# Performance work log

Hardware: AMD Instinct MI355X
Metric: run time of the kernel (lower is better)

The kernel has to match this reference:

```python
import jax, jax.numpy as jnp
import numpy as np

N_NODES = 100000
N_EDGES = 1600000
IN_FEATS = 256
HEADS = 4
OUT_FEATS = 32


def setup_inputs() -> dict:
    key = jax.random.key(0)
    k1, k2, k3, k4, k5, k6 = jax.random.split(key, 6)
    feat = jax.random.normal(k1, (N_NODES, IN_FEATS), dtype=jnp.float32)
    fc_w = jax.random.normal(k2, (HEADS * OUT_FEATS, IN_FEATS), dtype=jnp.float32) * (1.0 / np.sqrt(IN_FEATS))
    attn_l = jax.random.normal(k3, (1, HEADS, OUT_FEATS), dtype=jnp.float32) * 0.1
    attn_r = jax.random.normal(k4, (1, HEADS, OUT_FEATS), dtype=jnp.float32) * 0.1
    src = jax.random.randint(k5, (N_EDGES,), 0, N_NODES, dtype=jnp.int32)
    dst = jax.random.randint(k6, (N_EDGES,), 0, N_NODES, dtype=jnp.int32)
    return {"feat": feat, "fc_w": fc_w, "attn_l": attn_l, "attn_r": attn_r, "src": src, "dst": dst}


def reference(feat, fc_w, attn_l, attn_r, src, dst):
    # feat: [N, F_in]; fc_w: [H*D, F_in]; attn_l/r: [1, H, D]; src/dst: [E]
    N = feat.shape[0]
    H, D = attn_l.shape[1], attn_l.shape[2]
    # linear projection (no bias), viewed as [N, H, D]
    ft = (feat @ fc_w.T).reshape(N, H, D)
    # per-node attention logits
    el = jnp.einsum('nhd,hd->nh', ft, attn_l[0])  # [N, H]
    er = jnp.einsum('nhd,hd->nh', ft, attn_r[0])  # [N, H]
    # per-edge score: leaky_relu(el[src] + er[dst])
    e = jax.nn.leaky_relu(el[src] + er[dst], negative_slope=0.2)  # [E, H]
    # edge softmax over incoming edges of each dst node (stable)
    emax = jax.ops.segment_max(e, dst, num_segments=N)  # [N, H]
    a = jnp.exp(e - emax[dst])  # [E, H]
    asum = jax.ops.segment_sum(a, dst, num_segments=N)  # [N, H]
    a = a / asum[dst]
    # attn_drop is a no-op in eval mode; weighted scatter-sum aggregation
    msg = ft[src] * a[:, :, None]  # [E, H, D]
    out = jax.ops.segment_sum(msg, dst, num_segments=N)  # [N, H, D]
    # final_layer=False, activation=None, norm=None -> flatten heads
    return out.reshape(N, H * D)
```

## Files before the change

kernel.cpp:

```cpp
#include <hip/hip_runtime.h>
#include <hip/hip_bf16.h>
#include <float.h>

#define IN_F 256
#define HD   128
#define NH   4
#define GM   128

typedef __bf16 bf16x8 __attribute__((ext_vector_type(8)));
typedef __bf16 bf16x2 __attribute__((ext_vector_type(2)));
typedef float  f32x4  __attribute__((ext_vector_type(4)));

__device__ __forceinline__ bf16x8 cvt8(const float4 a, const float4 b) {
    bf16x8 r;
    r[0] = (__bf16)a.x; r[1] = (__bf16)a.y; r[2] = (__bf16)a.z; r[3] = (__bf16)a.w;
    r[4] = (__bf16)b.x; r[5] = (__bf16)b.y; r[6] = (__bf16)b.z; r[7] = (__bf16)b.w;
    return r;
}

__global__ __launch_bounds__(256) void gemm_ft_mfma(const float* __restrict__ feat,
                                                    const float* __restrict__ w,
                                                    __bf16* __restrict__ ft,
                                                    int N, int ntiles) {
    __shared__ __align__(16) __bf16 Bs[128][264];
    __shared__ __align__(16) __bf16 As[GM][40];
    const int t = threadIdx.x;
    const int wv = t >> 6;
    const int lane = t & 63;

    {
        const int col = t >> 1;
        const int koff = (t & 1) * 128;
        const float* wp = w + (size_t)col * IN_F + koff;
#pragma unroll
        for (int i = 0; i < 128; i += 8) {
            const float4 v0 = *(const float4*)(wp + i);
            const float4 v1 = *(const float4*)(wp + i + 4);
            *(bf16x8*)&Bs[col][koff + i] = cvt8(v0, v1);
        }
    }

    const int ar = t >> 1;
    const int ac = (t & 1) * 16;
    const int frow = lane & 15;
    const int fk   = (lane >> 4) * 8;

    for (int tile = blockIdx.x; tile < ntiles; tile += gridDim.x) {
        const int row0 = tile * GM;
        f32x4 acc[2][8];
#pragma unroll
        for (int mt = 0; mt < 2; ++mt)
#pragma unroll
            for (int ct = 0; ct < 8; ++ct) acc[mt][ct] = {0.f, 0.f, 0.f, 0.f};

        for (int ks = 0; ks < 8; ++ks) {
            const int k0 = ks * 32;
            __syncthreads();
            bf16x8 av0, av1;
            const int gr = row0 + ar;
            if (gr < N) {
                const float* fp = feat + (size_t)gr * IN_F + k0 + ac;
                const float4 v0 = *(const float4*)(fp);
                const float4 v1 = *(const float4*)(fp + 4);
                const float4 v2 = *(const float4*)(fp + 8);
                const float4 v3 = *(const float4*)(fp + 12);
                av0 = cvt8(v0, v1);
                av1 = cvt8(v2, v3);
            } else {
#pragma unroll
                for (int i = 0; i < 8; ++i) { av0[i] = (__bf16)0.f; av1[i] = (__bf16)0.f; }
            }
            *(bf16x8*)&As[ar][ac] = av0;
            *(bf16x8*)&As[ar][ac + 8] = av1;
            __syncthreads();

            const bf16x8 af0 = *(const bf16x8*)&As[wv * 32 + frow][fk];
            const bf16x8 af1 = *(const bf16x8*)&As[wv * 32 + 16 + frow][fk];
#pragma unroll
            for (int ct = 0; ct < 8; ++ct) {
                const bf16x8 bfrag = *(const bf16x8*)&Bs[ct * 16 + frow][k0 + fk];
                acc[0][ct] = __builtin_amdgcn_mfma_f32_16x16x32_bf16(af0, bfrag, acc[0][ct], 0, 0, 0);
                acc[1][ct] = __builtin_amdgcn_mfma_f32_16x16x32_bf16(af1, bfrag, acc[1][ct], 0, 0, 0);
            }
        }
        const int rb = row0 + wv * 32 + (lane >> 4) * 4;
#pragma unroll
        for (int mt = 0; mt < 2; ++mt)
#pragma unroll
            for (int ct = 0; ct < 8; ++ct)
#pragma unroll
                for (int reg = 0; reg < 4; ++reg) {
                    const int m = rb + mt * 16 + reg;
                    if (m < N) ft[(size_t)m * HD + ct * 16 + frow] = (__bf16)acc[mt][ct][reg];
                }
    }
}

__global__ __launch_bounds__(256) void eler_k(const __bf16* __restrict__ ft,
                                              const float* __restrict__ attn_l,
                                              const float* __restrict__ attn_r,
                                              float* __restrict__ el,
                                              float* __restrict__ er, int N) {
    const int lane = threadIdx.x & 63;
    const int node = blockIdx.x * 4 + (threadIdx.x >> 6);
    if (node >= N) return;
    const bf16x2 f  = *(const bf16x2*)(ft + (size_t)node * HD + lane * 2);
    const float2 al = *(const float2*)(attn_l + lane * 2);
    const float2 ar = *(const float2*)(attn_r + lane * 2);
    const float fx = (float)f[0], fy = (float)f[1];
    float pl = fx * al.x + fy * al.y;
    float pr = fx * ar.x + fy * ar.y;
#pragma unroll
    for (int s = 1; s < 16; s <<= 1) {
        pl += __shfl_xor(pl, s);
        pr += __shfl_xor(pr, s);
    }
    if ((lane & 15) == 0) {
        const int h = lane >> 4;
        el[(size_t)node * NH + h] = pl;
        er[(size_t)node * NH + h] = pr;
    }
}

__global__ __launch_bounds__(256) void deg_rank_k(const int* __restrict__ dst,
                                                  int* __restrict__ deg,
                                                  int* __restrict__ rank, int E) {
    const int i = blockIdx.x * 256 + threadIdx.x;
    if (i < E) rank[i] = atomicAdd(&deg[dst[i]], 1);
}

__global__ __launch_bounds__(1024) void scan1_k(const int* __restrict__ deg,
                                                int* __restrict__ off,
                                                int* __restrict__ bsum, int N) {
    __shared__ int lds[1024];
    const int t = threadIdx.x;
    const int g = blockIdx.x * 1024 + t;
    const int x = (g < N) ? deg[g] : 0;
    lds[t] = x;
    __syncthreads();
    int v = x;
    for (int s = 1; s < 1024; s <<= 1) {
        const int add = (t >= s) ? lds[t - s] : 0;
        __syncthreads();
        v += add;
        lds[t] = v;
        __syncthreads();
    }
    if (g < N) off[g] = v - x;
    if (t == 1023) bsum[blockIdx.x] = v;
}

__global__ __launch_bounds__(128) void scan2_k(const int* __restrict__ bsum,
                                               int* __restrict__ boff, int nb) {
    __shared__ int lds[128];
    const int t = threadIdx.x;
    const int x = (t < nb) ? bsum[t] : 0;
    lds[t] = x;
    __syncthreads();
    int v = x;
    for (int s = 1; s < 128; s <<= 1) {
        const int add = (t >= s) ? lds[t - s] : 0;
        __syncthreads();
        v += add;
        lds[t] = v;
        __syncthreads();
    }
    boff[t] = v - x;
}

__global__ __launch_bounds__(256) void scatter_k(const int* __restrict__ src,
                                                 const int* __restrict__ dst,
                                                 const int* __restrict__ off,
                                                 const int* __restrict__ boff,
                                                 const int* __restrict__ rank,
                                                 int* __restrict__ ssrc, int E) {
    const int i = blockIdx.x * 256 + threadIdx.x;
    if (i < E) {
        const int d = dst[i];
        const int p = off[d] + boff[d >> 10] + rank[i];
        ssrc[p] = src[i];
    }
}

__global__ __launch_bounds__(64) void aggregate_k(const __bf16* __restrict__ ft,
                                                  const float* __restrict__ el,
                                                  const float* __restrict__ er,
                                                  const int* __restrict__ deg,
                                                  const int* __restrict__ off,
                                                  const int* __restrict__ boff,
                                                  const int* __restrict__ ssrc,
                                                  float* __restrict__ out, int N) {
    const int n = blockIdx.x;
    const int lane = threadIdx.x;
    const int il = lane & 15;
    const int q  = lane >> 4;
    const int h  = il >> 2;
    float4* outp = (float4*)(out + (size_t)n * HD);
    const int dn = deg[n];
    if (dn == 0) {
        if (q < 2) outp[il * 2 + q] = make_float4(0.f, 0.f, 0.f, 0.f);
        return;
    }
    const int start = off[n] + boff[n >> 10];
    const float4 er4 = *(const float4*)(er + (size_t)n * NH);

    __shared__ float a_lds[64 * NH];
    __shared__ int   s_lds[64];
    float4 ssum = make_float4(0.f, 0.f, 0.f, 0.f);
    float acc[8];
#pragma unroll
    for (int i = 0; i < 8; ++i) acc[i] = 0.f;

    for (int c0 = 0; c0 < dn; c0 += 64) {
        const int j = c0 + lane;
        float4 a = make_float4(0.f, 0.f, 0.f, 0.f);
        int sv = 0;
        if (j < dn) {
            sv = ssrc[start + j];
            float4 e = *(const float4*)(el + (size_t)sv * NH);
            e.x += er4.x; e.y += er4.y; e.z += er4.z; e.w += er4.w;
            e.x = e.x >= 0.f ? e.x : 0.2f * e.x;
            e.y = e.y >= 0.f ? e.y : 0.2f * e.y;
            e.z = e.z >= 0.f ? e.z : 0.2f * e.z;
            e.w = e.w >= 0.f ? e.w : 0.2f * e.w;
            a.x = __expf(e.x); a.y = __expf(e.y);
            a.z = __expf(e.z); a.w = __expf(e.w);
            ssum.x += a.x; ssum.y += a.y; ssum.z += a.z; ssum.w += a.w;
        }
        s_lds[lane] = sv;
        *(float4*)(a_lds + lane * NH) = a;
        __syncthreads();
        const int cnt = min(64, dn - c0);
        for (int j2 = 0; j2 < cnt; j2 += 8) {
            const int e0 = j2 + q;
            const int e1 = j2 + 4 + q;
            const int sv0 = s_lds[e0];
            const int sv1 = s_lds[e1];
            const float a0 = a_lds[e0 * NH + h];
            const float a1 = a_lds[e1 * NH + h];
            const bf16x8 f0 = *(const bf16x8*)(ft + (size_t)sv0 * HD + il * 8);
            const bf16x8 f1 = *(const bf16x8*)(ft + (size_t)sv1 * HD + il * 8);
#pragma unroll
            for (int k = 0; k < 8; ++k) acc[k] = fmaf(a0, (float)f0[k], acc[k]);
#pragma unroll
            for (int k = 0; k < 8; ++k) acc[k] = fmaf(a1, (float)f1[k], acc[k]);
        }
        __syncthreads();
    }
#pragma unroll
    for (int s = 1; s < 64; s <<= 1) {
        ssum.x += __shfl_xor(ssum.x, s);
        ssum.y += __shfl_xor(ssum.y, s);
        ssum.z += __shfl_xor(ssum.z, s);
        ssum.w += __shfl_xor(ssum.w, s);
    }
#pragma unroll
    for (int k = 0; k < 8; ++k) {
        acc[k] += __shfl_xor(acc[k], 16);
        acc[k] += __shfl_xor(acc[k], 32);
    }
    const float sumh = (h == 0) ? ssum.x : (h == 1) ? ssum.y : (h == 2) ? ssum.z : ssum.w;
    const float inv = 1.f / sumh;
    if (q < 2) {
        const int b = q * 4;
        outp[il * 2 + q] = make_float4(acc[b] * inv, acc[b + 1] * inv,
                                       acc[b + 2] * inv, acc[b + 3] * inv);
    }
}

extern "C" void kernel_launch(void* const* d_in, const int* in_sizes, int n_in,
                              void* d_out, int out_size, void* d_ws, size_t ws_size,
                              hipStream_t stream) {
    const float* feat   = (const float*)d_in[0];
    const float* fc_w   = (const float*)d_in[1];
    const float* attn_l = (const float*)d_in[2];
    const float* attn_r = (const float*)d_in[3];
    const int*   src    = (const int*)d_in[4];
    const int*   dst    = (const int*)d_in[5];
    const int N = in_sizes[0] / IN_F;
    const int E = in_sizes[4];
    float* out = (float*)d_out;

    char* wp = (char*)d_ws;
    __bf16* ft = (__bf16*)wp; wp += (size_t)N * HD * 2;
    float* el  = (float*)wp; wp += (size_t)N * NH * 4;
    float* er  = (float*)wp; wp += (size_t)N * NH * 4;
    int* deg   = (int*)wp;   wp += (size_t)N * 4;
    int* off   = (int*)wp;   wp += (size_t)N * 4;
    int* bsum  = (int*)wp;   wp += 1024;
    int* boff  = (int*)wp;   wp += 1024;
    int* rank  = (int*)wp;   wp += (size_t)E * 4;
    int* ssrc  = (int*)wp;   wp += (size_t)E * 4;

    hipMemsetAsync(deg, 0, (size_t)N * 4, stream);

    const int ntiles = (N + GM - 1) / GM;
    gemm_ft_mfma<<<dim3(512), dim3(256), 0, stream>>>(feat, fc_w, ft, N, ntiles);
    eler_k<<<dim3((N + 3) / 4), dim3(256), 0, stream>>>(ft, attn_l, attn_r, el, er, N);
    deg_rank_k<<<dim3((E + 255) / 256), dim3(256), 0, stream>>>(dst, deg, rank, E);
    const int nblk = (N + 1023) >> 10;
    scan1_k<<<dim3(nblk), dim3(1024), 0, stream>>>(deg, off, bsum, N);
    scan2_k<<<dim3(1), dim3(128), 0, stream>>>(bsum, boff, nblk);
    scatter_k<<<dim3((E + 255) / 256), dim3(256), 0, stream>>>(src, dst, off, boff, rank, ssrc, E);
    aggregate_k<<<dim3(N), dim3(64), 0, stream>>>(ft, el, er, deg, off, boff, ssrc, out, N);
}
```

Baseline: 385.9 us.

## Fuse attention logits into LDS-free GEMM, warp-shuffle scan, unroll aggregation gathers

Weights are pre-converted once into bf16 MFMA fragment order by a small prep kernel. The projection GEMM then reads A fragments straight from global memory, with no LDS staging and no barriers, and computes el/er in its epilogue from the fp32 accumulators. This removes the separate eler kernel and its reread of ft. The block scan now uses wavefront shuffles instead of a barrier-heavy LDS Hillis-Steele loop, and the aggregation loop gathers four neighbor rows per step instead of two to raise memory-level parallelism. The risks are redundant global reads of feat and weight fragments across waves, and extra register pressure.

```diff
diff --git a/kernel.cpp b/kernel.cpp
--- a/kernel.cpp
+++ b/kernel.cpp
@@ -5,7 +5,6 @@
 #define IN_F 256
 #define HD   128
 #define NH   4
-#define GM   128
 
 typedef __bf16 bf16x8 __attribute__((ext_vector_type(8)));
 typedef __bf16 bf16x2 __attribute__((ext_vector_type(2)));
@@ -18,107 +17,108 @@
     return r;
 }
 
-__global__ __launch_bounds__(256) void gemm_ft_mfma(const float* __restrict__ feat,
-                                                    const float* __restrict__ w,
-                                                    __bf16* __restrict__ ft,
-                                                    int N, int ntiles) {
-    __shared__ __align__(16) __bf16 Bs[128][264];
-    __shared__ __align__(16) __bf16 As[GM][40];
+__global__ __launch_bounds__(256) void wprep_k(const float* __restrict__ w,
+                                               __bf16* __restrict__ wfrag) {
+    const int idx = blockIdx.x * 256 + threadIdx.x;
+    const int lane = idx & 63;
+    const int ct = (idx >> 6) & 7;
+    const int ks = idx >> 9;
+    const float* p = w + (size_t)(ct * 16 + (lane & 15)) * IN_F + ks * 32 + (lane >> 4) * 8;
+    const float4 v0 = *(const float4*)p;
+    const float4 v1 = *(const float4*)(p + 4);
+    *(bf16x8*)&wfrag[(size_t)idx * 8] = cvt8(v0, v1);
+}
+
+__global__ __launch_bounds__(256) void gemm_ft_fused(const float* __restrict__ feat,
+                                                     const __bf16* __restrict__ wfrag,
+                                                     const float* __restrict__ attn_l,
+                                                     const float* __restrict__ attn_r,
+                                                     __bf16* __restrict__ ft,
+                                                     float* __restrict__ el,
+                                                     float* __restrict__ er, int N) {
     const int t = threadIdx.x;
     const int wv = t >> 6;
     const int lane = t & 63;
-
-    {
-        const int col = t >> 1;
-        const int koff = (t & 1) * 128;
-        const float* wp = w + (size_t)col * IN_F + koff;
-#pragma unroll
-        for (int i = 0; i < 128; i += 8) {
-            const float4 v0 = *(const float4*)(wp + i);
-            const float4 v1 = *(const float4*)(wp + i + 4);
-            *(bf16x8*)&Bs[col][koff + i] = cvt8(v0, v1);
-        }
-    }
-
-    const int ar = t >> 1;
-    const int ac = (t & 1) * 16;
-    const int frow = lane & 15;
-    const int fk   = (lane >> 4) * 8;
-
-    for (int tile = blockIdx.x; tile < ntiles; tile += gridDim.x) {
-        const int row0 = tile * GM;
-        f32x4 acc[2][8];
-#pragma unroll
-        for (int mt = 0; mt < 2; ++mt)
-#pragma unroll
-            for (int ct = 0; ct < 8; ++ct) acc[mt][ct] = {0.f, 0.f, 0.f, 0.f};
-
-        for (int ks = 0; ks < 8; ++ks) {
-            const int k0 = ks * 32;
-            __syncthreads();
-            bf16x8 av0, av1;
-            const int gr = row0 + ar;
-            if (gr < N) {
-                const float* fp = feat + (size_t)gr * IN_F + k0 + ac;
-                const float4 v0 = *(const float4*)(fp);
-                const float4 v1 = *(const float4*)(fp + 4);
-                const float4 v2 = *(const float4*)(fp + 8);
-                const float4 v3 = *(const float4*)(fp + 12);
-                av0 = cvt8(v0, v1);
-                av1 = cvt8(v2, v3);
+    const int il = lane & 15;
+    const int fk = (lane >> 4) * 8;
+    const int rbase = blockIdx.x * 128 + wv * 32;
+
+    f32x4 acc[2][8];
+#pragma unroll
+    for (int mt = 0; mt < 2; ++mt)
+#pragma unroll
+        for (int ct = 0; ct < 8; ++ct) acc[mt][ct] = {0.f, 0.f, 0.f, 0.f};
+
+    const int r0 = rbase + il;
+    const int r1 = rbase + 16 + il;
+
+    for (int ks = 0; ks < 8; ++ks) {
+        bf16x8 af0, af1;
+        {
+            if (r0 < N) {
+                const float* p = feat + (size_t)r0 * IN_F + ks * 32 + fk;
+                af0 = cvt8(*(const float4*)p, *(const float4*)(p + 4));
             } else {
 #pragma unroll
-                for (int i = 0; i < 8; ++i) { av0[i] = (__bf16)0.f; av1[i] = (__bf16)0.f; }
-            }
-            *(bf16x8*)&As[ar][ac] = av0;
-            *(bf16x8*)&As[ar][ac + 8] = av1;
-            __syncthreads();
-
-            const bf16x8 af0 = *(const bf16x8*)&As[wv * 32 + frow][fk];
-            const bf16x8 af1 = *(const bf16x8*)&As[wv * 32 + 16 + frow][fk];
-#pragma unroll
-            for (int ct = 0; ct < 8; ++ct) {
-                const bf16x8 bfrag = *(const bf16x8*)&Bs[ct * 16 + frow][k0 + fk];
-                acc[0][ct] = __builtin_amdgcn_mfma_f32_16x16x32_bf16(af0, bfrag, acc[0][ct], 0, 0, 0);
-                acc[1][ct] = __builtin_amdgcn_mfma_f32_16x16x32_bf16(af1, bfrag, acc[1][ct], 0, 0, 0);
-            }
-        }
-        const int rb = row0 + wv * 32 + (lane >> 4) * 4;
-#pragma unroll
-        for (int mt = 0; mt < 2; ++mt)
+                for (int i = 0; i < 8; ++i) af0[i] = (__bf16)0.f;
+            }
+            if (r1 < N) {
+                const float* p = feat + (size_t)r1 * IN_F + ks * 32 + fk;
+                af1 = cvt8(*(const float4*)p, *(const float4*)(p + 4));
+            } else {
+#pragma unroll
+                for (int i = 0; i < 8; ++i) af1[i] = (__bf16)0.f;
+            }
+        }
+        const bf16x8* bp = (const bf16x8*)&wfrag[(size_t)(ks * 8) * 512 + lane * 8];
+#pragma unroll
+        for (int ct = 0; ct < 8; ++ct) {
+            const bf16x8 bfrag = bp[ct * 64];
+            acc[0][ct] = __builtin_amdgcn_mfma_f32_16x16x32_bf16(af0, bfrag, acc[0][ct], 0, 0, 0);
+            acc[1][ct] = __builtin_amdgcn_mfma_f32_16x16x32_bf16(af1, bfrag, acc[1][ct], 0, 0, 0);
+        }
+    }
+
+    float AL[8], AR[8];
+#pragma unroll
+    for (int ct = 0; ct < 8; ++ct) {
+        AL[ct] = attn_l[ct * 16 + il];
+        AR[ct] = attn_r[ct * 16 + il];
+    }
+
+    const int rquad = (lane >> 4) * 4;
+#pragma unroll
+    for (int mt = 0; mt < 2; ++mt) {
+#pragma unroll
+        for (int reg = 0; reg < 4; ++reg) {
+            const int row = rbase + mt * 16 + rquad + reg;
 #pragma unroll
             for (int ct = 0; ct < 8; ++ct)
-#pragma unroll
-                for (int reg = 0; reg < 4; ++reg) {
-                    const int m = rb + mt * 16 + reg;
-                    if (m < N) ft[(size_t)m * HD + ct * 16 + frow] = (__bf16)acc[mt][ct][reg];
+                if (row < N) ft[(size_t)row * HD + ct * 16 + il] = (__bf16)acc[mt][ct][reg];
+            float pl[NH], pr[NH];
+#pragma unroll
+            for (int h = 0; h < NH; ++h) {
+                const float v0 = acc[mt][2 * h][reg], v1 = acc[mt][2 * h + 1][reg];
+                pl[h] = v0 * AL[2 * h] + v1 * AL[2 * h + 1];
+                pr[h] = v0 * AR[2 * h] + v1 * AR[2 * h + 1];
+            }
+#pragma unroll
+            for (int s = 1; s < 16; s <<= 1) {
+#pragma unroll
+                for (int h = 0; h < NH; ++h) {
+                    pl[h] += __shfl_xor(pl[h], s);
+                    pr[h] += __shfl_xor(pr[h], s);
                 }
-    }
-}
-
-__global__ __launch_bounds__(256) void eler_k(const __bf16* __restrict__ ft,
-                                              const float* __restrict__ attn_l,
-                                              const float* __restrict__ attn_r,
-                                              float* __restrict__ el,
-                                              float* __restrict__ er, int N) {
-    const int lane = threadIdx.x & 63;
-    const int node = blockIdx.x * 4 + (threadIdx.x >> 6);
-    if (node >= N) return;
-    const bf16x2 f  = *(const bf16x2*)(ft + (size_t)node * HD + lane * 2);
-    const float2 al = *(const float2*)(attn_l + lane * 2);
-    const float2 ar = *(const float2*)(attn_r + lane * 2);
-    const float fx = (float)f[0], fy = (float)f[1];
-    float pl = fx * al.x + fy * al.y;
-    float pr = fx * ar.x + fy * ar.y;
-#pragma unroll
-    for (int s = 1; s < 16; s <<= 1) {
-        pl += __shfl_xor(pl, s);
-        pr += __shfl_xor(pr, s);
-    }
-    if ((lane & 15) == 0) {
-        const int h = lane >> 4;
-        el[(size_t)node * NH + h] = pl;
-        er[(size_t)node * NH + h] = pr;
+            }
+            if (il < 8 && row < N) {
+                const int h = il & 3;
+                const float v = (h == 0) ? ((il < 4) ? pl[0] : pr[0])
+                              : (h == 1) ? ((il < 4) ? pl[1] : pr[1])
+                              : (h == 2) ? ((il < 4) ? pl[2] : pr[2])
+                                         : ((il < 4) ? pl[3] : pr[3]);
+                ((il < 4) ? el : er)[(size_t)row * NH + h] = v;
+            }
+        }
     }
 }
 
@@ -132,22 +132,33 @@
 __global__ __launch_bounds__(1024) void scan1_k(const int* __restrict__ deg,
                                                 int* __restrict__ off,
                                                 int* __restrict__ bsum, int N) {
-    __shared__ int lds[1024];
+    __shared__ int wsum[16];
     const int t = threadIdx.x;
+    const int lane = t & 63;
+    const int wid = t >> 6;
     const int g = blockIdx.x * 1024 + t;
     const int x = (g < N) ? deg[g] : 0;
-    lds[t] = x;
+    int v = x;
+#pragma unroll
+    for (int s = 1; s < 64; s <<= 1) {
+        const int u = __shfl_up(v, s);
+        if (lane >= s) v += u;
+    }
+    if (lane == 63) wsum[wid] = v;
     __syncthreads();
-    int v = x;
-    for (int s = 1; s < 1024; s <<= 1) {
-        const int add = (t >= s) ? lds[t - s] : 0;
-        __syncthreads();
-        v += add;
-        lds[t] = v;
-        __syncthreads();
-    }
-    if (g < N) off[g] = v - x;
-    if (t == 1023) bsum[blockIdx.x] = v;
+    if (t < 16) {
+        int wv_ = wsum[t];
+#pragma unroll
+        for (int s = 1; s < 16; s <<= 1) {
+            const int u = __shfl_up(wv_, s);
+            if (t >= s) wv_ += u;
+        }
+        wsum[t] = wv_;
+    }
+    __syncthreads();
+    const int woff = wid ? wsum[wid - 1] : 0;
+    if (g < N) off[g] = woff + v - x;
+    if (t == 1023) bsum[blockIdx.x] = wsum[15];
 }
 
 __global__ __launch_bounds__(128) void scan2_k(const int* __restrict__ bsum,
@@ -230,20 +241,24 @@
         s_lds[lane] = sv;
         *(float4*)(a_lds + lane * NH) = a;
         __syncthreads();
-        const int cnt = min(64, dn - c0);
-        for (int j2 = 0; j2 < cnt; j2 += 8) {
-            const int e0 = j2 + q;
-            const int e1 = j2 + 4 + q;
-            const int sv0 = s_lds[e0];
-            const int sv1 = s_lds[e1];
-            const float a0 = a_lds[e0 * NH + h];
-            const float a1 = a_lds[e1 * NH + h];
+        const int cnt16 = (min(64, dn - c0) + 15) & ~15;
+        for (int j2 = 0; j2 < cnt16; j2 += 16) {
+            const int e0 = j2 + q, e1 = j2 + 4 + q, e2 = j2 + 8 + q, e3 = j2 + 12 + q;
+            const int sv0 = s_lds[e0], sv1 = s_lds[e1], sv2 = s_lds[e2], sv3 = s_lds[e3];
+            const float a0 = a_lds[e0 * NH + h], a1 = a_lds[e1 * NH + h];
+            const float a2 = a_lds[e2 * NH + h], a3 = a_lds[e3 * NH + h];
             const bf16x8 f0 = *(const bf16x8*)(ft + (size_t)sv0 * HD + il * 8);
             const bf16x8 f1 = *(const bf16x8*)(ft + (size_t)sv1 * HD + il * 8);
+            const bf16x8 f2 = *(const bf16x8*)(ft + (size_t)sv2 * HD + il * 8);
+            const bf16x8 f3 = *(const bf16x8*)(ft + (size_t)sv3 * HD + il * 8);
 #pragma unroll
             for (int k = 0; k < 8; ++k) acc[k] = fmaf(a0, (float)f0[k], acc[k]);
 #pragma unroll
             for (int k = 0; k < 8; ++k) acc[k] = fmaf(a1, (float)f1[k], acc[k]);
+#pragma unroll
+            for (int k = 0; k < 8; ++k) acc[k] = fmaf(a2, (float)f2[k], acc[k]);
+#pragma unroll
+            for (int k = 0; k < 8; ++k) acc[k] = fmaf(a3, (float)f3[k], acc[k]);
         }
         __syncthreads();
     }
@@ -282,7 +297,8 @@
     float* out = (float*)d_out;
 
     char* wp = (char*)d_ws;
-    __bf16* ft = (__bf16*)wp; wp += (size_t)N * HD * 2;
+    __bf16* ft = (__bf16*)wp;    wp += (size_t)N * HD * 2;
+    __bf16* wfrag = (__bf16*)wp; wp += 32768 * 2;
     float* el  = (float*)wp; wp += (size_t)N * NH * 4;
     float* er  = (float*)wp; wp += (size_t)N * NH * 4;
     int* deg   = (int*)wp;   wp += (size_t)N * 4;
@@ -294,9 +310,9 @@
 
     hipMemsetAsync(deg, 0, (size_t)N * 4, stream);
 
-    const int ntiles = (N + GM - 1) / GM;
-    gemm_ft_mfma<<<dim3(512), dim3(256), 0, stream>>>(feat, fc_w, ft, N, ntiles);
-    eler_k<<<dim3((N + 3) / 4), dim3(256), 0, stream>>>(ft, attn_l, attn_r, el, er, N);
+    wprep_k<<<dim3(16), dim3(256), 0, stream>>>(fc_w, wfrag);
+    gemm_ft_fused<<<dim3((N + 127) / 128), dim3(256), 0, stream>>>(
+        feat, wfrag, attn_l, attn_r, ft, el, er, N);
     deg_rank_k<<<dim3((E + 255) / 256), dim3(256), 0, stream>>>(dst, deg, rank, E);
     const int nblk = (N + 1023) >> 10;
     scan1_k<<<dim3(nblk), dim3(1024), 0, stream>>>(deg, off, bsum, N);
```

After: 394.7 us. 2.3% more time.
